# Optimization experiments

Measured on AMD Instinct MI355X. Metric: run time of the kernel, lower is better.

The kernel has to match this reference:

```python
import jax, jax.numpy as jnp
import numpy as np

EPS = 1e-4
HEAD_DIM = 64
MP_T = 0.3


def _mp_conv1x1(x, w):
    # Magnitude-preserving 1x1 conv: weight is normalized per output filter
    # (torch: normalize(w) / sqrt(fan_in), with normalize using
    #  alpha = sqrt(n.numel()/w.numel()) = 1/sqrt(fan_in)).
    O, I, kh, kw = w.shape
    fan_in = I * kh * kw
    n = jnp.sqrt(jnp.sum(w * w, axis=(1, 2, 3), keepdims=True))  # [O,1,1,1]
    alpha = 1.0 / np.sqrt(fan_in)
    wn = w / (EPS + alpha * n) / np.sqrt(fan_in)
    # 1x1 'same' conv == channel matmul
    return jnp.einsum('oi,bihw->bohw', wn[:, :, 0, 0], x)


def _pixel_norm(x):
    # torch pixel_norm with default dim=1: normalize over axis 1 (the heads axis
    # for q/k/v of shape [b, heads, seq, head_dim]) -- faithful to source.
    return x * jax.lax.rsqrt(jnp.mean(x * x, axis=1, keepdims=True) + EPS)


def setup_inputs() -> dict:
    key = jax.random.key(0)
    k1, k2, k3 = jax.random.split(key, 3)
    b, c, h, w = 16, 512, 32, 32
    return {
        'x': jax.random.normal(k1, (b, c, h, w), dtype=jnp.float32),
        'w_attn': jax.random.normal(k2, (3 * c, c, 1, 1), dtype=jnp.float32),
        'w_proj': jax.random.normal(k3, (c, c, 1, 1), dtype=jnp.float32),
    }


def reference(x, w_attn, w_proj):
    b, c, h, w = x.shape
    hd = HEAD_DIM
    nh = c // hd
    seq = h * w

    x_proj = _mp_conv1x1(x, w_attn)                      # [b, 3c, h, w]
    x_proj = x_proj.reshape(b, 3 * c, seq).transpose(0, 2, 1)  # [b, seq, 3c]
    q, k, v = jnp.split(x_proj, 3, axis=-1)              # each [b, seq, c]

    def to_heads(t):
        return t.reshape(b, seq, nh, hd).transpose(0, 2, 1, 3)  # [b, nh, seq, hd]

    q, k, v = _pixel_norm(to_heads(q)), _pixel_norm(to_heads(k)), _pixel_norm(to_heads(v))

    # scaled dot product attention (no mask)
    scale = 1.0 / np.sqrt(hd)
    scores = jnp.einsum('bnqd,bnkd->bnqk', q, k) * scale
    attn = jax.nn.softmax(scores, axis=-1)
    res = jnp.einsum('bnqk,bnkd->bnqd', attn, v)         # [b, nh, seq, hd]

    # transpose(-1,-2) then reshape(b, -1, h, w): [b, nh, hd, seq] -> [b, c, h, w]
    res = res.transpose(0, 1, 3, 2).reshape(b, c, h, w)
    res = _mp_conv1x1(res, w_proj)

    # mp_add(input, res, t=0.3)
    t = MP_T
    scale_add = np.sqrt(t * t + (1 - t) ** 2)
    return ((1 - t) * x + t * res) / scale_add
```

## Files before the change

### kernel.cpp

```cpp
#include <hip/hip_runtime.h>
#include <hip/hip_bf16.h>


typedef __attribute__((ext_vector_type(8))) short short8;
typedef __attribute__((ext_vector_type(8))) unsigned short ushort8;
typedef __attribute__((ext_vector_type(4))) float f32x4;
typedef __attribute__((ext_vector_type(16))) float f32x16;
typedef __attribute__((ext_vector_type(4))) unsigned int uint4_t;

__device__ inline unsigned short f2bf(float v) {
  __hip_bfloat16 h = __float2bfloat16(v);
  return *reinterpret_cast<unsigned short*>(&h);
}
__device__ inline float bf2f(unsigned short u) {
  return __uint_as_float((unsigned)u << 16);
}
__device__ inline unsigned cvt_pk(float lo, float hi) {
  unsigned r;
  asm("v_cvt_pk_bf16_f32 %0, %1, %2" : "=v"(r) : "v"(lo), "v"(hi));
  return r;
}
__device__ inline float fexp2(float x) {
#if __has_builtin(__builtin_amdgcn_exp2f)
  return __builtin_amdgcn_exp2f(x);
#else
  float r;
  asm("v_exp_f32 %0, %1\n\ts_nop 0" : "=v"(r) : "v"(x));
  return r;
#endif
}
__device__ inline float frsq(float x) {
#if __has_builtin(__builtin_amdgcn_rsqf)
  return __builtin_amdgcn_rsqf(x);
#else
  return rsqrtf(x);
#endif
}
__device__ inline void gload16(const void* g, void* l) {
  __builtin_amdgcn_global_load_lds(
      (const __attribute__((address_space(1))) unsigned int*)g,
      (__attribute__((address_space(3))) unsigned int*)l, 16, 0, 0);
}

__global__ __launch_bounds__(256) void prep_kernel(
    const float* __restrict__ wa, const float* __restrict__ wp,
    __hip_bfloat16* __restrict__ wna, __hip_bfloat16* __restrict__ wnp,
    const float* __restrict__ x, __hip_bfloat16* __restrict__ xt) {
  __shared__ __align__(16) unsigned short trans[64][68];
  __shared__ float wsum[4];
  int bid = blockIdx.x;
  int t = threadIdx.x;
  if (bid < 2048) {
    int o = bid;
    const float* src;
    __hip_bfloat16* dst;
    if (o < 1536) {
      int g = o >> 9, rem = o & 511, n = rem >> 6, d = rem & 63;
      int row = g * 512 + (d >> 4) * 128 + n * 16 + (d & 15);
      src = wa + (size_t)o * 512;
      dst = wna + (size_t)row * 512;
    } else {
      src = wp + (size_t)(o - 1536) * 512;
      dst = wnp + (size_t)(o - 1536) * 512;
    }
    float a = src[t], b = src[t + 256];
    float ss = a * a + b * b;
#pragma unroll
    for (int off = 32; off > 0; off >>= 1) ss += __shfl_down(ss, off, 64);
    if ((t & 63) == 0) wsum[t >> 6] = ss;
    __syncthreads();
    float tot = wsum[0] + wsum[1] + wsum[2] + wsum[3];
    float r = 1.0f / (sqrtf(tot) + 2.2627416997969522e-3f);
    dst[t] = __float2bfloat16(a * r);
    dst[t + 256] = __float2bfloat16(b * r);
    return;
  }
  int bid2 = bid - 2048;
  int s0 = (bid2 & 15) * 64;
  int c0 = ((bid2 >> 4) & 7) * 64;
  int b = bid2 >> 7;
  int sl = t & 63, cg = t >> 6;
  const float* src = x + (size_t)b * 524288 + (size_t)(c0 + cg * 16) * 1024 + s0 + sl;
#pragma unroll
  for (int i = 0; i < 16; i += 2) {
    float v0 = src[(size_t)i * 1024];
    float v1 = src[(size_t)(i + 1) * 1024];
    *(unsigned*)&trans[sl][cg * 16 + i] = (unsigned)f2bf(v0) | ((unsigned)f2bf(v1) << 16);
  }
  __syncthreads();
  int sw = t >> 2, cw = (t & 3) * 16;
  __hip_bfloat16* dst = xt + (size_t)b * 524288 + (size_t)(s0 + sw) * 512 + c0 + cw;
  uint2 r0 = *(uint2*)&trans[sw][cw + 0];
  uint2 r1 = *(uint2*)&trans[sw][cw + 4];
  uint2 r2 = *(uint2*)&trans[sw][cw + 8];
  uint2 r3 = *(uint2*)&trans[sw][cw + 12];
  uint4 o0 = {r0.x, r0.y, r1.x, r1.y};
  uint4 o1 = {r2.x, r2.y, r3.x, r3.y};
  *(uint4*)dst = o0;
  *(uint4*)((char*)dst + 16) = o1;
}

__global__ __launch_bounds__(256) void gemm_qkv(
    const __hip_bfloat16* __restrict__ A, const __hip_bfloat16* __restrict__ B,
    __hip_bfloat16* __restrict__ q_sd, __hip_bfloat16* __restrict__ k_sd,
    __hip_bfloat16* __restrict__ v_ds) {
  __shared__ __align__(16) char smem[65536];
  char* AlB = smem;
  char* BlB = smem + 32768;
  int t = threadIdx.x;
  int w = t >> 6, l = t & 63;
  int l15 = l & 15, lg = l >> 4;
  int wm = w >> 1, wn = w & 1;
  int bid = blockIdx.x;
  int xcd = bid & 7;
  int idx = bid >> 3;
  int b = xcd * 2 + (idx >= 96 ? 1 : 0);
  int r = idx >= 96 ? idx - 96 : idx;
  int mt = r >> 3;
  int n0 = (r & 7) * 128;
  int m0 = mt * 128;
  int g = mt >> 2, dq = mt & 3;

  const char* Ab = (const char*)A + (size_t)m0 * 1024;
  const char* Bb = (const char*)B + (size_t)b * 1048576 + (size_t)n0 * 1024;
  int rl = t >> 3;
  int soff = ((t & 7) * 16) ^ ((rl & 7) << 4);
  const char* asrc = Ab + (size_t)rl * 1024 + soff;
  const char* bsrc = Bb + (size_t)rl * 1024 + soff;

#define STAGE(bi, k0b)                                                       \
  do {                                                                       \
    _Pragma("unroll") for (int i = 0; i < 4; ++i) {                          \
      gload16(asrc + (size_t)i * 32768 + (k0b), AlB + (bi)*16384 + i * 4096 + w * 1024); \
      gload16(bsrc + (size_t)i * 32768 + (k0b), BlB + (bi)*16384 + i * 4096 + w * 1024); \
    }                                                                        \
  } while (0)

  f32x4 acc[4][4];
#pragma unroll
  for (int mi = 0; mi < 4; ++mi)
#pragma unroll
    for (int ni = 0; ni < 4; ++ni) acc[mi][ni] = (f32x4){0.f, 0.f, 0.f, 0.f};

  STAGE(0, 0);
  __syncthreads();

  for (int ks = 0; ks < 8; ++ks) {
    int buf = ks & 1;
    if (ks < 7) STAGE(buf ^ 1, (ks + 1) * 128);
    short8 af[4][2], bf[4][2];
#pragma unroll
    for (int mi = 0; mi < 4; ++mi) {
      int row = wm * 64 + mi * 16 + l15;
      int sw = (row & 7) << 4;
#pragma unroll
      for (int h = 0; h < 2; ++h)
        af[mi][h] = *(const short8*)(AlB + buf * 16384 + row * 128 + ((h * 64 + lg * 16) ^ sw));
    }
#pragma unroll
    for (int ni = 0; ni < 4; ++ni) {
      int row = wn * 64 + ni * 16 + l15;
      int sw = (row & 7) << 4;
#pragma unroll
      for (int h = 0; h < 2; ++h)
        bf[ni][h] = *(const short8*)(BlB + buf * 16384 + row * 128 + ((h * 64 + lg * 16) ^ sw));
    }
    __builtin_amdgcn_s_setprio(1);
#pragma unroll
    for (int mi = 0; mi < 4; ++mi)
#pragma unroll
      for (int ni = 0; ni < 4; ++ni) {
        acc[mi][ni] = __builtin_amdgcn_mfma_f32_16x16x32_bf16(af[mi][0], bf[ni][0], acc[mi][ni], 0, 0, 0);
        acc[mi][ni] = __builtin_amdgcn_mfma_f32_16x16x32_bf16(af[mi][1], bf[ni][1], acc[mi][ni], 0, 0, 0);
      }
    __builtin_amdgcn_s_setprio(0);
    if (ks < 7) __syncthreads();
  }
#undef STAGE

  __syncthreads();

  if (g < 2) {
    unsigned short(*LT)[136] = (unsigned short(*)[136])smem;
#pragma unroll
    for (int mi = 0; mi < 4; ++mi)
#pragma unroll
      for (int ni = 0; ni < 4; ++ni) {
        int sl = wn * 64 + ni * 16 + l15;
        int lr0 = wm * 64 + mi * 16 + lg * 4;
        *(unsigned*)&LT[sl][lr0] = cvt_pk(acc[mi][ni][0], acc[mi][ni][1]);
        *(unsigned*)&LT[sl][lr0 + 2] = cvt_pk(acc[mi][ni][2], acc[mi][ni][3]);
      }
    __syncthreads();
    int s = t >> 1, dd8 = (t & 1) * 8;
    ushort8 v[8];
#pragma unroll
    for (int n = 0; n < 8; ++n) v[n] = *(ushort8*)&LT[s][n * 16 + dd8];
    float f[8];
#pragma unroll
    for (int j = 0; j < 8; ++j) {
      float ss = 0.f;
#pragma unroll
      for (int n = 0; n < 8; ++n) { float xv = bf2f(v[n][j]); ss += xv * xv; }
      f[j] = frsq(ss * 0.125f + 1e-4f);
    }
    if (g == 0) {
#pragma unroll
      for (int j = 0; j < 8; ++j) f[j] *= 0.18033688011112042f;
    }
    unsigned short* dstb = (unsigned short*)(g ? k_sd : q_sd) +
        ((size_t)(b * 8) * 1024 + n0 + s) * 64 + dq * 16 + dd8;
#pragma unroll
    for (int n = 0; n < 8; ++n) {
      uint4 o;
      o.x = cvt_pk(bf2f(v[n][0]) * f[0], bf2f(v[n][1]) * f[1]);
      o.y = cvt_pk(bf2f(v[n][2]) * f[2], bf2f(v[n][3]) * f[3]);
      o.z = cvt_pk(bf2f(v[n][4]) * f[4], bf2f(v[n][5]) * f[5]);
      o.w = cvt_pk(bf2f(v[n][6]) * f[6], bf2f(v[n][7]) * f[7]);
      *(uint4*)(dstb + (size_t)n * 65536) = o;
    }
  } else {
    unsigned short(*L)[136] = (unsigned short(*)[136])smem;
#pragma unroll
    for (int mi = 0; mi < 4; ++mi)
#pragma unroll
      for (int ni = 0; ni < 4; ++ni) {
        int sl = wn * 64 + ni * 16 + l15;
        int lr0 = wm * 64 + mi * 16 + lg * 4;
#pragma unroll
        for (int rr = 0; rr < 4; ++rr) L[lr0 + rr][sl] = f2bf(acc[mi][ni][rr]);
      }
    __syncthreads();
    int dd = t >> 4, s0 = (t & 15) * 8;
    ushort8 v[8];
#pragma unroll
    for (int n = 0; n < 8; ++n) v[n] = *(ushort8*)&L[n * 16 + dd][s0];
    float f[8];
#pragma unroll
    for (int j = 0; j < 8; ++j) {
      float ss = 0.f;
#pragma unroll
      for (int n = 0; n < 8; ++n) { float xv = bf2f(v[n][j]); ss += xv * xv; }
      f[j] = frsq(ss * 0.125f + 1e-4f);
    }
    unsigned short* dstb = (unsigned short*)v_ds +
        ((size_t)(b * 8) * 64 + dq * 16 + dd) * 1024 + n0 + s0;
#pragma unroll
    for (int n = 0; n < 8; ++n) {
      uint4 o;
      o.x = cvt_pk(bf2f(v[n][0]) * f[0], bf2f(v[n][1]) * f[1]);
      o.y = cvt_pk(bf2f(v[n][2]) * f[2], bf2f(v[n][3]) * f[3]);
      o.z = cvt_pk(bf2f(v[n][4]) * f[4], bf2f(v[n][5]) * f[5]);
      o.w = cvt_pk(bf2f(v[n][6]) * f[6], bf2f(v[n][7]) * f[7]);
      *(uint4*)(dstb + (size_t)n * 65536) = o;
    }
  }
}

template <int MODE>
__global__ __launch_bounds__(256) void gemm_bf16(
    const __hip_bfloat16* __restrict__ A, const __hip_bfloat16* __restrict__ B,
    void* __restrict__ Outv, const float* __restrict__ resid, int M) {
  __shared__ __align__(16) char Al[2][16384];
  __shared__ __align__(16) char Bl[2][16384];
  int t = threadIdx.x;
  int w = t >> 6, l = t & 63;
  int l15 = l & 15, lg = l >> 4;
  int wm = w >> 1, wn = w & 1;
  int bid = blockIdx.x;
  int mt = M >> 7;
  int half = mt * 8;
  int xcd = bid & 7;
  int idx = bid >> 3;
  int b = xcd * 2 + (idx >= half ? 1 : 0);
  int r = idx >= half ? idx - half : idx;
  int m0 = (r >> 3) * 128, n0 = (r & 7) * 128;

  const char* Ab = (const char*)A + (size_t)m0 * 1024;
  const char* Bb = (const char*)B + (size_t)b * 1048576 + (size_t)n0 * 1024;
  int rl = t >> 3;
  int soff = ((t & 7) * 16) ^ ((rl & 7) << 4);
  const char* asrc = Ab + (size_t)rl * 1024 + soff;
  const char* bsrc = Bb + (size_t)rl * 1024 + soff;

#define STAGE(bi, k0b)                                                    \
  do {                                                                    \
    _Pragma("unroll") for (int i = 0; i < 4; ++i) {                       \
      gload16(asrc + (size_t)i * 32768 + (k0b), Al[bi] + i * 4096 + w * 1024); \
      gload16(bsrc + (size_t)i * 32768 + (k0b), Bl[bi] + i * 4096 + w * 1024); \
    }                                                                     \
  } while (0)

  f32x4 acc[4][4];
#pragma unroll
  for (int mi = 0; mi < 4; ++mi)
#pragma unroll
    for (int ni = 0; ni < 4; ++ni) acc[mi][ni] = (f32x4){0.f, 0.f, 0.f, 0.f};

  STAGE(0, 0);
  __syncthreads();

  for (int ks = 0; ks < 8; ++ks) {
    int buf = ks & 1;
    if (ks < 7) STAGE(buf ^ 1, (ks + 1) * 128);
    short8 af[4][2], bf[4][2];
#pragma unroll
    for (int mi = 0; mi < 4; ++mi) {
      int row = wm * 64 + mi * 16 + l15;
      int sw = (row & 7) << 4;
#pragma unroll
      for (int h = 0; h < 2; ++h)
        af[mi][h] = *(const short8*)(Al[buf] + row * 128 + ((h * 64 + lg * 16) ^ sw));
    }
#pragma unroll
    for (int ni = 0; ni < 4; ++ni) {
      int row = wn * 64 + ni * 16 + l15;
      int sw = (row & 7) << 4;
#pragma unroll
      for (int h = 0; h < 2; ++h)
        bf[ni][h] = *(const short8*)(Bl[buf] + row * 128 + ((h * 64 + lg * 16) ^ sw));
    }
    __builtin_amdgcn_s_setprio(1);
#pragma unroll
    for (int mi = 0; mi < 4; ++mi)
#pragma unroll
      for (int ni = 0; ni < 4; ++ni) {
        acc[mi][ni] = __builtin_amdgcn_mfma_f32_16x16x32_bf16(af[mi][0], bf[ni][0], acc[mi][ni], 0, 0, 0);
        acc[mi][ni] = __builtin_amdgcn_mfma_f32_16x16x32_bf16(af[mi][1], bf[ni][1], acc[mi][ni], 0, 0, 0);
      }
    __builtin_amdgcn_s_setprio(0);
    if (ks < 7) __syncthreads();
  }
#undef STAGE

  float* outb = (float*)Outv + (size_t)b * M * 1024;
  const float* rb = resid + (size_t)b * M * 1024;
#pragma unroll
  for (int mi = 0; mi < 4; ++mi) {
    int row = m0 + wm * 64 + mi * 16 + lg * 4;
#pragma unroll
    for (int rr = 0; rr < 4; ++rr) {
      float* orow = outb + (size_t)(row + rr) * 1024 + n0 + wn * 64 + l15;
      const float* rrow = rb + (size_t)(row + rr) * 1024 + n0 + wn * 64 + l15;
#pragma unroll
      for (int ni = 0; ni < 4; ++ni)
        orow[ni * 16] = 0.9191450300180578f * rrow[ni * 16] +
                        0.39391929857916763f * acc[mi][ni][rr];
    }
  }
}

__global__ __launch_bounds__(256, 8) void attn_mfma(
    const __hip_bfloat16* __restrict__ q_sd, const __hip_bfloat16* __restrict__ k_sd,
    const __hip_bfloat16* __restrict__ v_ds, __hip_bfloat16* __restrict__ y_t) {
  __shared__ __align__(16) char K_lds[2][8192];
  __shared__ __align__(16) char V_lds[2][8192];
  int t = threadIdx.x;
  int w = t >> 6, l = t & 63;
  int l31 = l & 31, h5 = l >> 5;
  int swV = (l31 & 7) << 4;
  int pl = (l31 & 0x13) | ((l31 & 4) << 1) | ((l31 & 8) >> 1);
  int swK = (pl & 7) << 4;
  int bn = blockIdx.x, qb = blockIdx.y;
  const char* qg = (const char*)(q_sd + (size_t)bn * 65536);
  const char* kg = (const char*)(k_sd + (size_t)bn * 65536);
  const char* vg = (const char*)(v_ds + (size_t)bn * 65536);

  int q = qb * 128 + w * 32 + l31;
  short8 bq[4];
#pragma unroll
  for (int j = 0; j < 4; ++j)
    bq[j] = *(const short8*)(qg + (size_t)q * 128 + j * 32 + h5 * 16);

  f32x16 o_acc[2];
#pragma unroll
  for (int r = 0; r < 16; ++r) { o_acc[0][r] = 0.f; o_acc[1][r] = 0.f; }
  float l_run = 0.f;

  int rowS = t >> 2;
  int coff = (t & 3) * 32;
  int swrS = (rowS & 7) << 4;
  {
    const char* ksrc = kg + (size_t)t * 32;
    const char* vsrc = vg + (size_t)rowS * 2048 + coff;
    uint4 a0 = *(const uint4*)(ksrc);
    uint4 a1 = *(const uint4*)(ksrc + 16);
    uint4 b0 = *(const uint4*)(vsrc);
    uint4 b1 = *(const uint4*)(vsrc + 16);
    *(uint4*)(K_lds[0] + ((t * 32) ^ swrS)) = a0;
    *(uint4*)(K_lds[0] + ((t * 32 + 16) ^ swrS)) = a1;
    *(uint4*)(V_lds[0] + ((t * 32) ^ swrS)) = b0;
    *(uint4*)(V_lds[0] + ((t * 32 + 16) ^ swrS)) = b1;
  }
  __syncthreads();

  for (int kb = 0; kb < 16; ++kb) {
    int buf = kb & 1;
    uint4 pk0, pk1, pv0, pv1;
    if (kb < 15) {
      const char* ksrc = kg + (size_t)(kb + 1) * 8192 + (size_t)t * 32;
      const char* vsrc = vg + (size_t)rowS * 2048 + (size_t)(kb + 1) * 128 + coff;
      pk0 = *(const uint4*)(ksrc);
      pk1 = *(const uint4*)(ksrc + 16);
      pv0 = *(const uint4*)(vsrc);
      pv1 = *(const uint4*)(vsrc + 16);
    }
    short8 a_k[2][4];
#pragma unroll
    for (int kt = 0; kt < 2; ++kt)
#pragma unroll
      for (int j = 0; j < 4; ++j)
        a_k[kt][j] = *(const short8*)(K_lds[buf] +
            (((kt * 32 + pl) * 128 + j * 32 + h5 * 16) ^ swK));
    f32x16 s0, s1;
#pragma unroll
    for (int r = 0; r < 16; ++r) { s0[r] = 0.f; s1[r] = 0.f; }
    __builtin_amdgcn_s_setprio(1);
#pragma unroll
    for (int j = 0; j < 4; ++j) {
      s0 = __builtin_amdgcn_mfma_f32_32x32x16_bf16(a_k[0][j], bq[j], s0, 0, 0, 0);
      s1 = __builtin_amdgcn_mfma_f32_32x32x16_bf16(a_k[1][j], bq[j], s1, 0, 0, 0);
    }
    __builtin_amdgcn_s_setprio(0);
    unsigned W0[8], W1[8];
    float ts = 0.f;
#pragma unroll
    for (int m = 0; m < 8; ++m) {
      float p0 = fexp2(s0[2 * m]), p1 = fexp2(s0[2 * m + 1]);
      float p2 = fexp2(s1[2 * m]), p3 = fexp2(s1[2 * m + 1]);
      ts += (p0 + p1) + (p2 + p3);
      W0[m] = cvt_pk(p0, p1);
      W1[m] = cvt_pk(p2, p3);
    }
    l_run += ts;
    short8 pb[4];
#pragma unroll
    for (int j = 0; j < 4; ++j) {
      uint4_t pw;
      if (j == 0)      pw = (uint4_t){W0[0], W0[1], W0[2], W0[3]};
      else if (j == 1) pw = (uint4_t){W0[4], W0[5], W0[6], W0[7]};
      else if (j == 2) pw = (uint4_t){W1[0], W1[1], W1[2], W1[3]};
      else             pw = (uint4_t){W1[4], W1[5], W1[6], W1[7]};
      pb[j] = __builtin_bit_cast(short8, pw);
    }
    short8 a_v[2][4];
#pragma unroll
    for (int dt = 0; dt < 2; ++dt)
#pragma unroll
      for (int j = 0; j < 4; ++j)
        a_v[dt][j] = *(const short8*)(V_lds[buf] +
            (((dt * 32 + l31) * 128 + j * 32 + h5 * 16) ^ swV));
    __builtin_amdgcn_s_setprio(1);
#pragma unroll
    for (int j = 0; j < 4; ++j) {
      o_acc[0] = __builtin_amdgcn_mfma_f32_32x32x16_bf16(a_v[0][j], pb[j], o_acc[0], 0, 0, 0);
      o_acc[1] = __builtin_amdgcn_mfma_f32_32x32x16_bf16(a_v[1][j], pb[j], o_acc[1], 0, 0, 0);
    }
    __builtin_amdgcn_s_setprio(0);
    if (kb < 15) {
      int nb = buf ^ 1;
      *(uint4*)(K_lds[nb] + ((t * 32) ^ swrS)) = pk0;
      *(uint4*)(K_lds[nb] + ((t * 32 + 16) ^ swrS)) = pk1;
      *(uint4*)(V_lds[nb] + ((t * 32) ^ swrS)) = pv0;
      *(uint4*)(V_lds[nb] + ((t * 32 + 16) ^ swrS)) = pv1;
    }
    __syncthreads();
  }
  int b_ = bn >> 3, n_ = bn & 7;
  float lsum = l_run + __shfl_xor(l_run, 32, 64);
  float invl = 1.0f / lsum;
  __hip_bfloat16* yrow = y_t + (size_t)b_ * 524288 + (size_t)q * 512 + n_ * 64 + h5 * 4;
#pragma unroll
  for (int dt = 0; dt < 2; ++dt) {
#pragma unroll
    for (int g4 = 0; g4 < 4; ++g4) {
      uint2 pr;
      pr.x = cvt_pk(o_acc[dt][4 * g4 + 0] * invl, o_acc[dt][4 * g4 + 1] * invl);
      pr.y = cvt_pk(o_acc[dt][4 * g4 + 2] * invl, o_acc[dt][4 * g4 + 3] * invl);
      *(uint2*)(yrow + dt * 32 + g4 * 8) = pr;
    }
  }
}

extern "C" void kernel_launch(void* const* d_in, const int* in_sizes, int n_in,
                              void* d_out, int out_size, void* d_ws, size_t ws_size,
                              hipStream_t stream) {
  const float* x      = (const float*)d_in[0];
  const float* w_attn = (const float*)d_in[1];
  const float* w_proj = (const float*)d_in[2];
  float* out = (float*)d_out;

  __hip_bfloat16* wn_attn = (__hip_bfloat16*)d_ws;
  __hip_bfloat16* wn_proj = wn_attn + 786432;
  __hip_bfloat16* x_t     = wn_proj + 262144;
  __hip_bfloat16* y_t     = x_t;
  __hip_bfloat16* q_sd    = x_t + 8388608;
  __hip_bfloat16* k_sd    = q_sd + 8388608;
  __hip_bfloat16* v_ds    = k_sd + 8388608;

  prep_kernel<<<dim3(4096), dim3(256), 0, stream>>>(w_attn, w_proj, wn_attn, wn_proj, x, x_t);
  gemm_qkv<<<dim3(1536), dim3(256), 0, stream>>>(wn_attn, x_t, q_sd, k_sd, v_ds);
  attn_mfma<<<dim3(128, 8), dim3(256), 0, stream>>>(q_sd, k_sd, v_ds, y_t);
  gemm_bf16<1><<<dim3(512), dim3(256), 0, stream>>>(wn_proj, y_t, out, x, 512);
}
```

Measured before the change: 126.6 us.

## Use direct global-to-LDS loads and 512-thread attention blocks covering 256 queries

The attention kernel now runs 512 threads per block, so each block handles 256 queries instead of 128 and each K/V tile loaded into LDS serves twice as many queries. K/V staging switches from register-staged global loads followed by LDS stores to a gload16 direct global-to-LDS path with pre-swizzled source addresses. This removes the register round trip and the store phase at the end of each iteration. The cost is fewer, larger blocks (512 total) and lower occupancy per CU via launch bounds 4.

```diff
diff --git a/kernel.cpp b/kernel.cpp
--- a/kernel.cpp
+++ b/kernel.cpp
@@ -350,7 +350,7 @@
   }
 }
 
-__global__ __launch_bounds__(256, 8) void attn_mfma(
+__global__ __launch_bounds__(512, 4) void attn_mfma(
     const __hip_bfloat16* __restrict__ q_sd, const __hip_bfloat16* __restrict__ k_sd,
     const __hip_bfloat16* __restrict__ v_ds, __hip_bfloat16* __restrict__ y_t) {
   __shared__ __align__(16) char K_lds[2][8192];
@@ -366,7 +366,7 @@
   const char* kg = (const char*)(k_sd + (size_t)bn * 65536);
   const char* vg = (const char*)(v_ds + (size_t)bn * 65536);
 
-  int q = qb * 128 + w * 32 + l31;
+  int q = qb * 256 + w * 32 + l31;
   short8 bq[4];
 #pragma unroll
   for (int j = 0; j < 4; ++j)
@@ -377,33 +377,25 @@
   for (int r = 0; r < 16; ++r) { o_acc[0][r] = 0.f; o_acc[1][r] = 0.f; }
   float l_run = 0.f;
 
-  int rowS = t >> 2;
-  int coff = (t & 3) * 32;
-  int swrS = (rowS & 7) << 4;
-  {
-    const char* ksrc = kg + (size_t)t * 32;
-    const char* vsrc = vg + (size_t)rowS * 2048 + coff;
-    uint4 a0 = *(const uint4*)(ksrc);
-    uint4 a1 = *(const uint4*)(ksrc + 16);
-    uint4 b0 = *(const uint4*)(vsrc);
-    uint4 b1 = *(const uint4*)(vsrc + 16);
-    *(uint4*)(K_lds[0] + ((t * 32) ^ swrS)) = a0;
-    *(uint4*)(K_lds[0] + ((t * 32 + 16) ^ swrS)) = a1;
-    *(uint4*)(V_lds[0] + ((t * 32) ^ swrS)) = b0;
-    *(uint4*)(V_lds[0] + ((t * 32 + 16) ^ swrS)) = b1;
-  }
+  int p = t * 16;
+  int psw = ((p >> 7) & 7) << 4;
+  int qoff = p ^ psw;
+  const char* ksrc0 = kg + qoff;
+  const char* vsrc0 = vg + (size_t)(p >> 7) * 2048 + (qoff & 127);
+  char* kdst0 = K_lds[0] + w * 1024;
+  char* kdst1 = K_lds[1] + w * 1024;
+  char* vdst0 = V_lds[0] + w * 1024;
+  char* vdst1 = V_lds[1] + w * 1024;
+  gload16(ksrc0, kdst0);
+  gload16(vsrc0, vdst0);
   __syncthreads();
 
+#pragma unroll 2
   for (int kb = 0; kb < 16; ++kb) {
     int buf = kb & 1;
-    uint4 pk0, pk1, pv0, pv1;
     if (kb < 15) {
-      const char* ksrc = kg + (size_t)(kb + 1) * 8192 + (size_t)t * 32;
-      const char* vsrc = vg + (size_t)rowS * 2048 + (size_t)(kb + 1) * 128 + coff;
-      pk0 = *(const uint4*)(ksrc);
-      pk1 = *(const uint4*)(ksrc + 16);
-      pv0 = *(const uint4*)(vsrc);
-      pv1 = *(const uint4*)(vsrc + 16);
+      gload16(ksrc0 + (size_t)(kb + 1) * 8192, buf ? kdst0 : kdst1);
+      gload16(vsrc0 + (size_t)(kb + 1) * 128, buf ? vdst0 : vdst1);
     }
     short8 a_k[2][4];
 #pragma unroll
@@ -457,13 +449,6 @@
       o_acc[1] = __builtin_amdgcn_mfma_f32_32x32x16_bf16(a_v[1][j], pb[j], o_acc[1], 0, 0, 0);
     }
     __builtin_amdgcn_s_setprio(0);
-    if (kb < 15) {
-      int nb = buf ^ 1;
-      *(uint4*)(K_lds[nb] + ((t * 32) ^ swrS)) = pk0;
-      *(uint4*)(K_lds[nb] + ((t * 32 + 16) ^ swrS)) = pk1;
-      *(uint4*)(V_lds[nb] + ((t * 32) ^ swrS)) = pv0;
-      *(uint4*)(V_lds[nb] + ((t * 32 + 16) ^ swrS)) = pv1;
-    }
     __syncthreads();
   }
   int b_ = bn >> 3, n_ = bn & 7;
@@ -500,6 +485,6 @@
 
   prep_kernel<<<dim3(4096), dim3(256), 0, stream>>>(w_attn, w_proj, wn_attn, wn_proj, x, x_t);
   gemm_qkv<<<dim3(1536), dim3(256), 0, stream>>>(wn_attn, x_t, q_sd, k_sd, v_ds);
-  attn_mfma<<<dim3(128, 8), dim3(256), 0, stream>>>(q_sd, k_sd, v_ds, y_t);
+  attn_mfma<<<dim3(128, 4), dim3(512), 0, stream>>>(q_sd, k_sd, v_ds, y_t);
   gemm_bf16<1><<<dim3(512), dim3(256), 0, stream>>>(wn_proj, y_t, out, x, 512);
 }
```

Result: slower. 151.9 us (+19.9%).
